# Optimization experiments

Measured on AMD Instinct MI355X. Metric: run time of the kernel, lower is better.

## Reference

```python
import jax, jax.numpy as jnp
import numpy as np

B, T, U, H = 4, 256, 64, 512
INNER, VOCAB = 512, 1024


def setup_inputs() -> dict:
    key = jax.random.key(0)
    ks = jax.random.split(key, 6)
    s_in = 1.0 / np.sqrt(2 * H)
    s_h = 1.0 / np.sqrt(INNER)
    return {
        "enc_state": jax.random.normal(ks[0], (B, T, H), dtype=jnp.float32),
        "dec_state": jax.random.normal(ks[1], (B, U, H), dtype=jnp.float32),
        "W1": jax.random.normal(ks[2], (2 * H, INNER), dtype=jnp.float32) * s_in,
        "b1": jnp.zeros((INNER,), dtype=jnp.float32),
        "W2": jax.random.normal(ks[3], (INNER, VOCAB), dtype=jnp.float32) * s_h,
        "b2": jnp.zeros((VOCAB,), dtype=jnp.float32),
    }


def reference(enc_state, dec_state, W1, b1, W2, b2):
    # JointNet: broadcast enc [B,T,1,H] and dec [B,1,U,H], concat -> Linear -> tanh -> Linear -> log_softmax
    # concat+Linear is split into two smaller matmuls (mathematically identical):
    # cat([e,d]) @ W1 == e @ W1[:H] + d @ W1[H:]
    enc_proj = jnp.einsum("bth,hi->bti", enc_state, W1[:H])      # [B,T,INNER]
    dec_proj = jnp.einsum("buh,hi->bui", dec_state, W1[H:])      # [B,U,INNER]
    hidden = jnp.tanh(enc_proj[:, :, None, :] + dec_proj[:, None, :, :] + b1)  # [B,T,U,INNER]
    logits = jnp.einsum("btui,iv->btuv", hidden, W2) + b2        # [B,T,U,VOCAB]
    return jax.nn.log_softmax(logits, axis=-1)
```

## Files before the change

### kernel.cpp

```cpp
#include <hip/hip_runtime.h>
#include <hip/hip_bf16.h>
#include <cstdint>
#include <cstddef>


typedef __attribute__((ext_vector_type(8))) short short8;
typedef __attribute__((ext_vector_type(4))) float f32x4;

#define BS_CHUNK 65536

#define WS_EP_OFF 0
#define WS_DP_OFF (1024 * 512 * 4)
#define WS_W2_OFF (WS_DP_OFF + 256 * 512 * 4)

#define SMEM_RED_OFF 65536
#define SMEM_TOTAL (65536 + 4096)

__device__ __forceinline__ unsigned short f2bf(float x) {
  unsigned int u = __builtin_bit_cast(unsigned int, x);
  u += 0x7FFFu + ((u >> 16) & 1u);
  return (unsigned short)(u >> 16);
}

__device__ __forceinline__ float fast_tanh(float x) {
  float ax = fabsf(x);
  float e = __expf(-2.0f * ax);
  float t = (1.0f - e) / (1.0f + e);
  return copysignf(t, x);
}

__global__ __launch_bounds__(512) void prep(
    const float* __restrict__ enc, const float* __restrict__ dec,
    const float* __restrict__ W1, const float* __restrict__ b1,
    const float* __restrict__ W2,
    float* __restrict__ ep, float* __restrict__ dp, char* __restrict__ w2st) {
  __shared__ float As[4 * 512];
  const int tid = threadIdx.x;
  if (blockIdx.x < 320) {
    const int r0 = blockIdx.x * 4;
    const bool isenc = (r0 < 1024);
    const float* A = isenc ? (enc + (size_t)r0 * 512) : (dec + (size_t)(r0 - 1024) * 512);
    const float* W = isenc ? W1 : (W1 + 512 * 512);
    float* O = isenc ? (ep + (size_t)r0 * 512) : (dp + (size_t)(r0 - 1024) * 512);

    for (int idx = tid; idx < 4 * 512; idx += 512) As[idx] = A[idx];
    __syncthreads();

    const int c = tid;
    float acc[4] = {0.f, 0.f, 0.f, 0.f};
    const float4* As4 = (const float4*)As;
#pragma unroll 4
    for (int k4 = 0; k4 < 128; ++k4) {
      const int kb = k4 * 4;
      float w0 = W[(size_t)(kb + 0) * 512 + c];
      float w1 = W[(size_t)(kb + 1) * 512 + c];
      float w2 = W[(size_t)(kb + 2) * 512 + c];
      float w3 = W[(size_t)(kb + 3) * 512 + c];
#pragma unroll
      for (int r = 0; r < 4; ++r) {
        float4 a = As4[r * 128 + k4];
        acc[r] += a.x * w0 + a.y * w1 + a.z * w2 + a.w * w3;
      }
    }
    const float bias = isenc ? b1[c] : 0.0f;
#pragma unroll
    for (int r = 0; r < 4; ++r) O[(size_t)r * 512 + c] = acc[r] + bias;
  } else {
    const int g = (blockIdx.x - 320) * 512 + tid;
    const int v = g & 1023;
    const int kc = g >> 10;
    unsigned short vals[32];
#pragma unroll
    for (int ki = 0; ki < 32; ++ki)
      vals[ki] = f2bf(W2[(size_t)(kc * 32 + ki) * 1024 + v]);
    uint4* dst = (uint4*)(w2st + (size_t)kc * BS_CHUNK + (size_t)v * 64);
    const uint4* s = (const uint4*)vals;
    dst[0] = s[0]; dst[1] = s[1]; dst[2] = s[2]; dst[3] = s[3];
  }
}

__global__ __launch_bounds__(512, 2) void joint(
    const float* __restrict__ ep, const float* __restrict__ dp,
    const char* __restrict__ w2st, const float* __restrict__ b2,
    float* __restrict__ out) {
  extern __shared__ char smem[];
  char* As = smem;
  float* redM = (float*)(smem + SMEM_RED_OFF);
  float* redS = redM + 512;

  const int tid = threadIdx.x;
  const int wave = tid >> 6, lane = tid & 63;
  const int lo = lane & 15, hi = lane >> 4;
  const int bt = blockIdx.x;
  const int m0 = bt * 64;
  const int dprow0 = (bt >> 8) * 64;
  const int nbase = wave * 128;

  const char* bbase = w2st + (size_t)(nbase + lo) * 64 + hi * 16;

  short8 b[8];
#pragma unroll
  for (int ni = 0; ni < 8; ++ni) b[ni] = *(const short8*)(bbase + ni * 1024);

  {
    const int c0 = (tid & 63) * 8;
    const int rb = tid >> 6;
    const float* epr = ep + (size_t)bt * 512 + c0;
    float e0[8];
    *(float4*)(e0) = *(const float4*)(epr);
    *(float4*)(e0 + 4) = *(const float4*)(epr + 4);
#pragma unroll
    for (int p = 0; p < 8; ++p) {
      const int row = rb + p * 8;
      const float* dpr = dp + (size_t)(dprow0 + row) * 512 + c0;
      float d0[8];
      *(float4*)(d0) = *(const float4*)(dpr);
      *(float4*)(d0 + 4) = *(const float4*)(dpr + 4);
      unsigned short h[8];
#pragma unroll
      for (int j = 0; j < 8; ++j) h[j] = f2bf(fast_tanh(e0[j] + d0[j]));
      *(uint4*)(As + ((row * 1024 + c0 * 2) ^ ((row & 7) << 4))) = *(const uint4*)h;
    }
  }

  f32x4 acc[4][8];
#pragma unroll
  for (int mi = 0; mi < 4; ++mi)
#pragma unroll
    for (int ni = 0; ni < 8; ++ni)
#pragma unroll
      for (int j = 0; j < 4; ++j) acc[mi][ni][j] = 0.0f;

  __syncthreads();

  const int axor = (lo & 7) << 4;

  for (int kc = 0; kc < 16; ++kc) {
    short8 bn[8];
    if (kc < 15) {
      const char* src = bbase + (size_t)(kc + 1) * BS_CHUNK;
#pragma unroll
      for (int ni = 0; ni < 8; ++ni) bn[ni] = *(const short8*)(src + ni * 1024);
    }
    short8 a[4];
#pragma unroll
    for (int mi = 0; mi < 4; ++mi)
      a[mi] = *(const short8*)(As + (((mi * 16 + lo) * 1024 + kc * 64 + hi * 16) ^ axor));
    __builtin_amdgcn_s_setprio(1);
#pragma unroll
    for (int ni = 0; ni < 8; ++ni)
#pragma unroll
      for (int mi = 0; mi < 4; ++mi)
        acc[mi][ni] = __builtin_amdgcn_mfma_f32_16x16x32_bf16(a[mi], b[ni], acc[mi][ni], 0, 0, 0);
    __builtin_amdgcn_s_setprio(0);
    if (kc < 15) {
#pragma unroll
      for (int ni = 0; ni < 8; ++ni) b[ni] = bn[ni];
    }
  }

  float b2v[8];
#pragma unroll
  for (int ni = 0; ni < 8; ++ni) b2v[ni] = b2[nbase + ni * 16 + lo];
#pragma unroll
  for (int mi = 0; mi < 4; ++mi)
#pragma unroll
    for (int ni = 0; ni < 8; ++ni)
#pragma unroll
      for (int j = 0; j < 4; ++j) acc[mi][ni][j] += b2v[ni];

  float pm[4][4];
#pragma unroll
  for (int mi = 0; mi < 4; ++mi)
#pragma unroll
    for (int r = 0; r < 4; ++r) {
      float m = -3.402823e38f;
#pragma unroll
      for (int ni = 0; ni < 8; ++ni) m = fmaxf(m, acc[mi][ni][r]);
      pm[mi][r] = m;
    }
#pragma unroll
  for (int off = 1; off < 16; off <<= 1)
#pragma unroll
    for (int mi = 0; mi < 4; ++mi)
#pragma unroll
      for (int r = 0; r < 4; ++r)
        pm[mi][r] = fmaxf(pm[mi][r], __shfl_xor(pm[mi][r], off));
  if (lo == 0) {
#pragma unroll
    for (int mi = 0; mi < 4; ++mi)
#pragma unroll
      for (int r = 0; r < 4; ++r)
        redM[wave * 64 + mi * 16 + hi * 4 + r] = pm[mi][r];
  }
  __syncthreads();
  float rm[4][4];
#pragma unroll
  for (int mi = 0; mi < 4; ++mi)
#pragma unroll
    for (int r = 0; r < 4; ++r) {
      const int row = mi * 16 + hi * 4 + r;
      float m = redM[row];
#pragma unroll
      for (int w = 1; w < 8; ++w) m = fmaxf(m, redM[w * 64 + row]);
      rm[mi][r] = m;
    }

  float ps[4][4];
#pragma unroll
  for (int mi = 0; mi < 4; ++mi)
#pragma unroll
    for (int r = 0; r < 4; ++r) {
      float s = 0.0f;
#pragma unroll
      for (int ni = 0; ni < 8; ++ni) s += __expf(acc[mi][ni][r] - rm[mi][r]);
      ps[mi][r] = s;
    }
#pragma unroll
  for (int off = 1; off < 16; off <<= 1)
#pragma unroll
    for (int mi = 0; mi < 4; ++mi)
#pragma unroll
      for (int r = 0; r < 4; ++r)
        ps[mi][r] += __shfl_xor(ps[mi][r], off);
  if (lo == 0) {
#pragma unroll
    for (int mi = 0; mi < 4; ++mi)
#pragma unroll
      for (int r = 0; r < 4; ++r)
        redS[wave * 64 + mi * 16 + hi * 4 + r] = ps[mi][r];
  }
  __syncthreads();

#pragma unroll
  for (int mi = 0; mi < 4; ++mi)
#pragma unroll
    for (int r = 0; r < 4; ++r) {
      const int row = mi * 16 + hi * 4 + r;
      float s = 0.0f;
#pragma unroll
      for (int w = 0; w < 8; ++w) s += redS[w * 64 + row];
      const float sub = rm[mi][r] + __logf(s);
      float* op = out + (size_t)(m0 + row) * 1024 + nbase + lo;
#pragma unroll
      for (int ni = 0; ni < 8; ++ni) op[ni * 16] = acc[mi][ni][r] - sub;
    }
}

extern "C" void kernel_launch(void* const* d_in, const int* in_sizes, int n_in,
                              void* d_out, int out_size, void* d_ws, size_t ws_size,
                              hipStream_t stream) {
  const float* enc = (const float*)d_in[0];
  const float* dec = (const float*)d_in[1];
  const float* W1  = (const float*)d_in[2];
  const float* b1  = (const float*)d_in[3];
  const float* W2  = (const float*)d_in[4];
  const float* b2  = (const float*)d_in[5];
  float* out = (float*)d_out;

  char* ws = (char*)d_ws;
  float* ep = (float*)(ws + WS_EP_OFF);
  float* dp = (float*)(ws + WS_DP_OFF);
  char* w2st = ws + WS_W2_OFF;

  prep<<<352, 512, 0, stream>>>(enc, dec, W1, b1, W2, ep, dp, w2st);
  joint<<<1024, 512, SMEM_TOTAL, stream>>>(ep, dp, w2st, b2, out);
}
```

Before: 180.5 us.

## Widen joint kernel to 16 waves with rotated K order and two-stage softmax reduction

The joint kernel now runs 1024 threads (16 waves), each wave owning 64 vocab columns instead of 128. This halves per-wave accumulator and B-fragment registers so more waves can hide latency. Each block starts its K loop at a different chunk (bt&15) to spread reads of the staged W2 across L2/memory. The cross-wave max and sum reductions become a shuffle-based second stage through extra LDS. The prep kernel processes 8 rows per block, and tanh uses a hardware reciprocal instead of a divide. The risk is that 64 KB of LDS per block still caps residency, and the extra barriers add overhead.

```diff
diff --git a/kernel.cpp b/kernel.cpp
--- a/kernel.cpp
+++ b/kernel.cpp
@@ -13,8 +13,7 @@
 #define WS_DP_OFF (1024 * 512 * 4)
 #define WS_W2_OFF (WS_DP_OFF + 256 * 512 * 4)
 
-#define SMEM_RED_OFF 65536
-#define SMEM_TOTAL (65536 + 4096)
+#define SMEM_TOTAL (65536 + 4096 + 256 + 4096 + 256)
 
 __device__ __forceinline__ unsigned short f2bf(float x) {
   unsigned int u = __builtin_bit_cast(unsigned int, x);
@@ -25,7 +24,7 @@
 __device__ __forceinline__ float fast_tanh(float x) {
   float ax = fabsf(x);
   float e = __expf(-2.0f * ax);
-  float t = (1.0f - e) / (1.0f + e);
+  float t = (1.0f - e) * __builtin_amdgcn_rcpf(1.0f + e);
   return copysignf(t, x);
 }
 
@@ -34,22 +33,24 @@
     const float* __restrict__ W1, const float* __restrict__ b1,
     const float* __restrict__ W2,
     float* __restrict__ ep, float* __restrict__ dp, char* __restrict__ w2st) {
-  __shared__ float As[4 * 512];
+  __shared__ float As[8 * 512];
   const int tid = threadIdx.x;
-  if (blockIdx.x < 320) {
-    const int r0 = blockIdx.x * 4;
+  if (blockIdx.x < 160) {
+    const int r0 = blockIdx.x * 8;
     const bool isenc = (r0 < 1024);
     const float* A = isenc ? (enc + (size_t)r0 * 512) : (dec + (size_t)(r0 - 1024) * 512);
     const float* W = isenc ? W1 : (W1 + 512 * 512);
     float* O = isenc ? (ep + (size_t)r0 * 512) : (dp + (size_t)(r0 - 1024) * 512);
 
-    for (int idx = tid; idx < 4 * 512; idx += 512) As[idx] = A[idx];
+    for (int idx = tid; idx < 8 * 512; idx += 512) As[idx] = A[idx];
     __syncthreads();
 
     const int c = tid;
-    float acc[4] = {0.f, 0.f, 0.f, 0.f};
+    float acc[8];
+#pragma unroll
+    for (int r = 0; r < 8; ++r) acc[r] = 0.0f;
     const float4* As4 = (const float4*)As;
-#pragma unroll 4
+#pragma unroll 2
     for (int k4 = 0; k4 < 128; ++k4) {
       const int kb = k4 * 4;
       float w0 = W[(size_t)(kb + 0) * 512 + c];
@@ -57,16 +58,16 @@
       float w2 = W[(size_t)(kb + 2) * 512 + c];
       float w3 = W[(size_t)(kb + 3) * 512 + c];
 #pragma unroll
-      for (int r = 0; r < 4; ++r) {
+      for (int r = 0; r < 8; ++r) {
         float4 a = As4[r * 128 + k4];
         acc[r] += a.x * w0 + a.y * w1 + a.z * w2 + a.w * w3;
       }
     }
     const float bias = isenc ? b1[c] : 0.0f;
 #pragma unroll
-    for (int r = 0; r < 4; ++r) O[(size_t)r * 512 + c] = acc[r] + bias;
+    for (int r = 0; r < 8; ++r) O[(size_t)r * 512 + c] = acc[r] + bias;
   } else {
-    const int g = (blockIdx.x - 320) * 512 + tid;
+    const int g = (blockIdx.x - 160) * 512 + tid;
     const int v = g & 1023;
     const int kc = g >> 10;
     unsigned short vals[32];
@@ -79,14 +80,16 @@
   }
 }
 
-__global__ __launch_bounds__(512, 2) void joint(
+__global__ __launch_bounds__(1024, 4) void joint(
     const float* __restrict__ ep, const float* __restrict__ dp,
     const char* __restrict__ w2st, const float* __restrict__ b2,
     float* __restrict__ out) {
   extern __shared__ char smem[];
   char* As = smem;
-  float* redM = (float*)(smem + SMEM_RED_OFF);
-  float* redS = redM + 512;
+  float* redM = (float*)(smem + 65536);
+  float* redF = redM + 1024;
+  float* redS = redF + 64;
+  float* redF2 = redS + 1024;
 
   const int tid = threadIdx.x;
   const int wave = tid >> 6, lane = tid & 63;
@@ -94,24 +97,28 @@
   const int bt = blockIdx.x;
   const int m0 = bt * 64;
   const int dprow0 = (bt >> 8) * 64;
-  const int nbase = wave * 128;
+  const int nbase = wave * 64;
+  const int krot = bt & 15;
 
   const char* bbase = w2st + (size_t)(nbase + lo) * 64 + hi * 16;
 
-  short8 b[8];
-#pragma unroll
-  for (int ni = 0; ni < 8; ++ni) b[ni] = *(const short8*)(bbase + ni * 1024);
+  short8 b[4];
+  {
+    const char* src = bbase + (size_t)krot * BS_CHUNK;
+#pragma unroll
+    for (int ni = 0; ni < 4; ++ni) b[ni] = *(const short8*)(src + ni * 1024);
+  }
 
   {
     const int c0 = (tid & 63) * 8;
-    const int rb = tid >> 6;
+    const int rg = tid >> 6;
     const float* epr = ep + (size_t)bt * 512 + c0;
     float e0[8];
     *(float4*)(e0) = *(const float4*)(epr);
     *(float4*)(e0 + 4) = *(const float4*)(epr + 4);
 #pragma unroll
-    for (int p = 0; p < 8; ++p) {
-      const int row = rb + p * 8;
+    for (int p = 0; p < 4; ++p) {
+      const int row = rg + p * 16;
       const float* dpr = dp + (size_t)(dprow0 + row) * 512 + c0;
       float d0[8];
       *(float4*)(d0) = *(const float4*)(dpr);
@@ -123,49 +130,54 @@
     }
   }
 
-  f32x4 acc[4][8];
-#pragma unroll
-  for (int mi = 0; mi < 4; ++mi)
-#pragma unroll
-    for (int ni = 0; ni < 8; ++ni)
+  f32x4 acc[4][4];
+#pragma unroll
+  for (int mi = 0; mi < 4; ++mi)
+#pragma unroll
+    for (int ni = 0; ni < 4; ++ni)
 #pragma unroll
       for (int j = 0; j < 4; ++j) acc[mi][ni][j] = 0.0f;
 
   __syncthreads();
 
-  const int axor = (lo & 7) << 4;
-
+#pragma unroll 1
   for (int kc = 0; kc < 16; ++kc) {
-    short8 bn[8];
+    int kci = kc + krot;
+    kci = (kci >= 16) ? kci - 16 : kci;
+    short8 bn[4];
     if (kc < 15) {
-      const char* src = bbase + (size_t)(kc + 1) * BS_CHUNK;
-#pragma unroll
-      for (int ni = 0; ni < 8; ++ni) bn[ni] = *(const short8*)(src + ni * 1024);
+      int kn = kci + 1;
+      kn = (kn >= 16) ? 0 : kn;
+      const char* src = bbase + (size_t)kn * BS_CHUNK;
+#pragma unroll
+      for (int ni = 0; ni < 4; ++ni) bn[ni] = *(const short8*)(src + ni * 1024);
     }
     short8 a[4];
 #pragma unroll
-    for (int mi = 0; mi < 4; ++mi)
-      a[mi] = *(const short8*)(As + (((mi * 16 + lo) * 1024 + kc * 64 + hi * 16) ^ axor));
+    for (int mi = 0; mi < 4; ++mi) {
+      const int row = mi * 16 + lo;
+      a[mi] = *(const short8*)(As + ((row * 1024 + kci * 64 + hi * 16) ^ ((row & 7) << 4)));
+    }
     __builtin_amdgcn_s_setprio(1);
 #pragma unroll
-    for (int ni = 0; ni < 8; ++ni)
+    for (int ni = 0; ni < 4; ++ni)
 #pragma unroll
       for (int mi = 0; mi < 4; ++mi)
         acc[mi][ni] = __builtin_amdgcn_mfma_f32_16x16x32_bf16(a[mi], b[ni], acc[mi][ni], 0, 0, 0);
     __builtin_amdgcn_s_setprio(0);
     if (kc < 15) {
 #pragma unroll
-      for (int ni = 0; ni < 8; ++ni) b[ni] = bn[ni];
-    }
-  }
-
-  float b2v[8];
-#pragma unroll
-  for (int ni = 0; ni < 8; ++ni) b2v[ni] = b2[nbase + ni * 16 + lo];
-#pragma unroll
-  for (int mi = 0; mi < 4; ++mi)
-#pragma unroll
-    for (int ni = 0; ni < 8; ++ni)
+      for (int ni = 0; ni < 4; ++ni) b[ni] = bn[ni];
+    }
+  }
+
+  float b2v[4];
+#pragma unroll
+  for (int ni = 0; ni < 4; ++ni) b2v[ni] = b2[nbase + ni * 16 + lo];
+#pragma unroll
+  for (int mi = 0; mi < 4; ++mi)
+#pragma unroll
+    for (int ni = 0; ni < 4; ++ni)
 #pragma unroll
       for (int j = 0; j < 4; ++j) acc[mi][ni][j] += b2v[ni];
 
@@ -174,9 +186,8 @@
   for (int mi = 0; mi < 4; ++mi)
 #pragma unroll
     for (int r = 0; r < 4; ++r) {
-      float m = -3.402823e38f;
-#pragma unroll
-      for (int ni = 0; ni < 8; ++ni) m = fmaxf(m, acc[mi][ni][r]);
+      float m = fmaxf(fmaxf(acc[mi][0][r], acc[mi][1][r]),
+                      fmaxf(acc[mi][2][r], acc[mi][3][r]));
       pm[mi][r] = m;
     }
 #pragma unroll
@@ -194,56 +205,63 @@
         redM[wave * 64 + mi * 16 + hi * 4 + r] = pm[mi][r];
   }
   __syncthreads();
+  {
+    const int tr = tid >> 4, w = tid & 15;
+    float v = redM[w * 64 + tr];
+#pragma unroll
+    for (int off = 1; off < 16; off <<= 1) v = fmaxf(v, __shfl_xor(v, off));
+    if (w == 0) redF[tr] = v;
+  }
+  __syncthreads();
   float rm[4][4];
+#pragma unroll
+  for (int mi = 0; mi < 4; ++mi)
+#pragma unroll
+    for (int r = 0; r < 4; ++r) rm[mi][r] = redF[mi * 16 + hi * 4 + r];
+
+  float ps[4][4];
+#pragma unroll
+  for (int mi = 0; mi < 4; ++mi)
+#pragma unroll
+    for (int r = 0; r < 4; ++r) {
+      float s = 0.0f;
+#pragma unroll
+      for (int ni = 0; ni < 4; ++ni) s += __expf(acc[mi][ni][r] - rm[mi][r]);
+      ps[mi][r] = s;
+    }
+#pragma unroll
+  for (int off = 1; off < 16; off <<= 1)
+#pragma unroll
+    for (int mi = 0; mi < 4; ++mi)
+#pragma unroll
+      for (int r = 0; r < 4; ++r)
+        ps[mi][r] += __shfl_xor(ps[mi][r], off);
+  if (lo == 0) {
+#pragma unroll
+    for (int mi = 0; mi < 4; ++mi)
+#pragma unroll
+      for (int r = 0; r < 4; ++r)
+        redS[wave * 64 + mi * 16 + hi * 4 + r] = ps[mi][r];
+  }
+  __syncthreads();
+  {
+    const int tr = tid >> 4, w = tid & 15;
+    float v = redS[w * 64 + tr];
+#pragma unroll
+    for (int off = 1; off < 16; off <<= 1) v += __shfl_xor(v, off);
+    if (w == 0) redF2[tr] = v;
+  }
+  __syncthreads();
+
 #pragma unroll
   for (int mi = 0; mi < 4; ++mi)
 #pragma unroll
     for (int r = 0; r < 4; ++r) {
       const int row = mi * 16 + hi * 4 + r;
-      float m = redM[row];
-#pragma unroll
-      for (int w = 1; w < 8; ++w) m = fmaxf(m, redM[w * 64 + row]);
-      rm[mi][r] = m;
-    }
-
-  float ps[4][4];
-#pragma unroll
-  for (int mi = 0; mi < 4; ++mi)
-#pragma unroll
-    for (int r = 0; r < 4; ++r) {
-      float s = 0.0f;
-#pragma unroll
-      for (int ni = 0; ni < 8; ++ni) s += __expf(acc[mi][ni][r] - rm[mi][r]);
-      ps[mi][r] = s;
-    }
-#pragma unroll
-  for (int off = 1; off < 16; off <<= 1)
-#pragma unroll
-    for (int mi = 0; mi < 4; ++mi)
-#pragma unroll
-      for (int r = 0; r < 4; ++r)
-        ps[mi][r] += __shfl_xor(ps[mi][r], off);
-  if (lo == 0) {
-#pragma unroll
-    for (int mi = 0; mi < 4; ++mi)
-#pragma unroll
-      for (int r = 0; r < 4; ++r)
-        redS[wave * 64 + mi * 16 + hi * 4 + r] = ps[mi][r];
-  }
-  __syncthreads();
-
-#pragma unroll
-  for (int mi = 0; mi < 4; ++mi)
-#pragma unroll
-    for (int r = 0; r < 4; ++r) {
-      const int row = mi * 16 + hi * 4 + r;
-      float s = 0.0f;
-#pragma unroll
-      for (int w = 0; w < 8; ++w) s += redS[w * 64 + row];
-      const float sub = rm[mi][r] + __logf(s);
+      const float sub = rm[mi][r] + __logf(redF2[row]);
       float* op = out + (size_t)(m0 + row) * 1024 + nbase + lo;
 #pragma unroll
-      for (int ni = 0; ni < 8; ++ni) op[ni * 16] = acc[mi][ni][r] - sub;
+      for (int ni = 0; ni < 4; ++ni) op[ni * 16] = acc[mi][ni][r] - sub;
     }
 }
 
@@ -263,6 +281,6 @@
   float* dp = (float*)(ws + WS_DP_OFF);
   char* w2st = ws + WS_W2_OFF;
 
-  prep<<<352, 512, 0, stream>>>(enc, dec, W1, b1, W2, ep, dp, w2st);
-  joint<<<1024, 512, SMEM_TOTAL, stream>>>(ep, dp, w2st, b2, out);
-}
+  prep<<<192, 512, 0, stream>>>(enc, dec, W1, b1, W2, ep, dp, w2st);
+  joint<<<1024, 1024, SMEM_TOTAL, stream>>>(ep, dp, w2st, b2, out);
+}
```

Result: slower. 190.3 us (+5.4%).
